# Kernel optimization log

Measured on AMD Instinct MI355X. Metric: run time of the kernel, lower is better.

## Reference

```python
import jax, jax.numpy as jnp
import numpy as np
from jax import lax

B, N, D = 2, 2048, 256
S, DC, E = 16, 4, 2
DI = E * D            # d_inner = 512
DTR = (D + 15) // 16  # dt_rank = 16


def layernorm(x, w, b):
    m = x.mean(-1, keepdims=True)
    v = ((x - m) ** 2).mean(-1, keepdims=True)
    return (x - m) / jnp.sqrt(v + 1e-5) * w + b


def mamba_block(x, in_w, conv_w, conv_b, xproj_w, dt_w, dt_b, A_log, Dp, out_w):
    # x: [B, N, D]
    xz = jnp.einsum('bnd,ed->bne', x, in_w)          # [B,N,2*DI]
    xc, z = jnp.split(xz, 2, axis=-1)
    # depthwise causal conv1d, kernel DC, left-pad DC-1
    xpad = jnp.pad(xc, ((0, 0), (DC - 1, 0), (0, 0)))
    xconv = sum(xpad[:, k:k + N, :] * conv_w[:, k] for k in range(DC)) + conv_b
    xa = jax.nn.silu(xconv)                           # [B,N,DI]
    x_dbl = jnp.einsum('bnd,ed->bne', xa, xproj_w)    # [B,N,DTR+2S]
    dt = x_dbl[..., :DTR]
    Bm = x_dbl[..., DTR:DTR + S]                      # [B,N,S]
    Cm = x_dbl[..., DTR + S:]                         # [B,N,S]
    dt = jax.nn.softplus(jnp.einsum('bnr,dr->bnd', dt, dt_w) + dt_b)  # [B,N,DI]
    A = -jnp.exp(A_log)                               # [DI,S]
    dA = jnp.exp(dt[..., None] * A)                   # [B,N,DI,S]
    dBu = dt[..., None] * Bm[:, :, None, :] * xa[..., None]

    def step(h, inp):
        dA_t, dBu_t, C_t = inp
        h = dA_t * h + dBu_t                          # [B,DI,S]
        y = jnp.einsum('bds,bs->bd', h, C_t)
        return h, y

    h0 = jnp.zeros((x.shape[0], DI, S), dtype=x.dtype)
    _, ys = lax.scan(step, h0, (dA.transpose(1, 0, 2, 3), dBu.transpose(1, 0, 2, 3), Cm.transpose(1, 0, 2)))
    y = ys.transpose(1, 0, 2) + xa * Dp               # skip D*u
    y = y * jax.nn.silu(z)
    return jnp.einsum('bnd,ed->bne', y, out_w)        # [B,N,D]


def stream_fwd(x, nw, nb, in_w, conv_w, conv_b, xproj_w, dt_w, dt_b, A_log, Dp, out_w):
    return x + mamba_block(layernorm(x, nw, nb), in_w, conv_w, conv_b, xproj_w, dt_w, dt_b, A_log, Dp, out_w)


def setup_inputs() -> dict:
    key = jax.random.key(0)
    ks = jax.random.split(key, 24)
    s = 0.02
    inp = {
        'edge_features': jax.random.normal(ks[0], (B, N, D), jnp.float32),
        'blob_features': jax.random.normal(ks[1], (B, N, D), jnp.float32),
        'spectral_features': jax.random.normal(ks[2], (B, N, D), jnp.float32),
        'norm_w': jnp.ones((3, D)),
        'norm_b': jnp.zeros((3, D)),
        'in_w': jax.random.normal(ks[3], (3, 2 * DI, D)) * s,
        'conv_w': jax.random.normal(ks[4], (3, DI, DC)) * s,
        'conv_b': jnp.zeros((3, DI)),
        'xproj_w': jax.random.normal(ks[5], (3, DTR + 2 * S, DI)) * s,
        'dt_w': jax.random.normal(ks[6], (3, DI, DTR)) * s,
        'dt_b': jax.random.uniform(ks[7], (3, DI), minval=-4.0, maxval=-2.0),
        'A_log': jnp.tile(jnp.log(jnp.arange(1, S + 1, dtype=jnp.float32)), (3, DI, 1)),
        'Dp': jnp.ones((3, DI)),
        'out_w': jax.random.normal(ks[8], (3, D, DI)) * s,
        'temperature': jnp.ones((1,)) * 0.1,
        'agg_w1': jax.random.normal(ks[9], (D, 3 * D)) * s,
        'agg_b1': jnp.zeros((D,)),
        'agg_w2': jax.random.normal(ks[10], (3, D)) * s,
        'agg_b2': jnp.zeros((3,)),
        'proj_w': jax.random.normal(ks[11], (D, 3 * D)) * s,
        'proj_b': jnp.zeros((D,)),
    }
    return inp


def reference(edge_features, blob_features, spectral_features, norm_w, norm_b, in_w,
              conv_w, conv_b, xproj_w, dt_w, dt_b, A_log, Dp, out_w, temperature,
              agg_w1, agg_b1, agg_w2, agg_b2, proj_w, proj_b):
    streams = jnp.stack([edge_features, blob_features, spectral_features])  # [3,B,N,D]
    proc = jax.vmap(stream_fwd)(streams, norm_w, norm_b, in_w, conv_w, conv_b,
                                xproj_w, dt_w, dt_b, A_log, Dp, out_w)      # [3,B,N,D]
    edge_p, blob_p, spec_p = proc[0], proc[1], proc[2]
    multi = jnp.concatenate([edge_p, blob_p, spec_p], axis=-1)              # [B,N,3D]
    pooled = multi.mean(axis=1, keepdims=True)                              # [B,1,3D]
    h = jax.nn.gelu(jnp.einsum('bne,de->bnd', pooled, agg_w1) + agg_b1)
    coeffs = jax.nn.softmax(jnp.einsum('bnd,kd->bnk', h, agg_w2) + agg_b2, axis=-1)
    coeffs = jax.nn.softmax(coeffs / (temperature + 1e-6), axis=-1)         # [B,1,3]
    weighted = (coeffs[:, :, 0:1] * edge_p + coeffs[:, :, 1:2] * blob_p +
                coeffs[:, :, 2:3] * spec_p)
    out = jnp.einsum('bne,de->bnd', multi, proj_w) + proj_b + weighted
    return out  # dropout is identity in eval
```

## Files before the change

kernel.cpp:

```cpp
#include <hip/hip_runtime.h>
#include <hip/hip_bf16.h>

#define NB 2
#define NN 2048
#define ND 256
#define NS 16
#define NDC 4
#define NDI 512
#define NDTR 16
#define LCH 64
#define NCH 32

typedef __hip_bfloat16 bf16;
typedef __attribute__((ext_vector_type(8))) __bf16 bf16x8;
typedef __attribute__((ext_vector_type(4))) float f32x4;

__device__ __forceinline__ float b2f(bf16 h) { return __bfloat162float(h); }

__device__ __forceinline__ void dec8(const uint4 u, float w[8]) {
    union { unsigned u; float f; } c;
    c.u = u.x << 16;          w[0] = c.f;
    c.u = u.x & 0xffff0000u;  w[1] = c.f;
    c.u = u.y << 16;          w[2] = c.f;
    c.u = u.y & 0xffff0000u;  w[3] = c.f;
    c.u = u.z << 16;          w[4] = c.f;
    c.u = u.z & 0xffff0000u;  w[5] = c.f;
    c.u = u.w << 16;          w[6] = c.f;
    c.u = u.w & 0xffff0000u;  w[7] = c.f;
}

struct CvtArgs { const void* s[21]; };
__device__ __constant__ const int seg_cum[22] = {
    0, 1048576, 2097152, 3145728, 3146496, 3147264, 3933696, 3939840,
    3941376, 4015104, 4039680, 4041216, 4065792, 4067328, 4460544, 4460545,
    4657153, 4657409, 4658177, 4658180, 4854788, 4855044 };
__device__ __constant__ const int seg_dst[21] = {
    0,        1048576,  2097152,  4847616, 4848384, 3145728, 4841472, 4849152, 4325376,
    4399104,  4850688,  4423680,  4852224, 3932160, 4855056, 4448256, 4853760, 4854016,
    4854784,  4644864,  4854800 };

__global__ __launch_bounds__(256) void k_convert(CvtArgs a, int* __restrict__ flag,
                                                 bf16* __restrict__ dst,
                                                 float* __restrict__ pooled)
{
    int idx = blockIdx.x * 256 + threadIdx.x;
    unsigned v0 = ((const unsigned*)a.s[3])[0];
    int f = ((v0 & 0xFFFFu) == 0u) ? 1 : 0;
    if (idx == 0) flag[0] = f;
    if (idx < 1536) pooled[idx] = 0.0f;
    if (idx >= 4855044) return;
    int seg = 0;
    #pragma unroll
    for (int i = 1; i < 21; i++) if (idx >= seg_cum[i]) seg = i;
    int off = idx - seg_cum[seg];
    bf16 v;
    if (f) v = __float2bfloat16(((const float*)a.s[seg])[off]);
    else   v = ((const bf16*)a.s[seg])[off];
    dst[seg_dst[seg] + off] = v;
}

__global__ __launch_bounds__(256) void k_layernorm(
    const bf16* __restrict__ e, const bf16* __restrict__ bl, const bf16* __restrict__ sp,
    const bf16* __restrict__ nw, const bf16* __restrict__ nb, bf16* __restrict__ xn)
{
    int row = blockIdx.x;
    int sb = row >> 11, n = row & (NN - 1);
    int s = sb >> 1, b = sb & 1;
    const bf16* xin = (s == 0) ? e : ((s == 1) ? bl : sp);
    int t = threadIdx.x;
    float v = b2f(xin[((b << 11) + n) * ND + t]);
    float s1 = v, s2 = v * v;
    #pragma unroll
    for (int m = 1; m < 64; m <<= 1) { s1 += __shfl_xor(s1, m); s2 += __shfl_xor(s2, m); }
    __shared__ float r1[4], r2[4];
    int w = t >> 6;
    if ((t & 63) == 0) { r1[w] = s1; r2[w] = s2; }
    __syncthreads();
    float mean = (r1[0] + r1[1] + r1[2] + r1[3]) * (1.0f / ND);
    float ms   = (r2[0] + r2[1] + r2[2] + r2[3]) * (1.0f / ND);
    float inv = rsqrtf(ms - mean * mean + 1e-5f);
    float wv = b2f(nw[s * ND + t]), bv = b2f(nb[s * ND + t]);
    xn[row * ND + t] = __float2bfloat16((v - mean) * inv * wv + bv);
}

__global__ __launch_bounds__(256) void k_inproj_t(
    const bf16* __restrict__ xn, const bf16* __restrict__ in_w,
    bf16* __restrict__ xc, bf16* __restrict__ z)
{
    __shared__ bf16 As[128 * 72];
    __shared__ bf16 Bs[128 * 72];
    int bid = blockIdx.x;
    int bm = bid >> 3, bn = bid & 7;
    int m0 = bm * 128, e0 = bn * 128;
    int s = m0 >> 12;
    const bf16* W = in_w + (size_t)s * (2 * NDI) * ND;
    int t = threadIdx.x;
    int w = t >> 6, l = t & 63;
    int wm = w >> 1, wn = w & 1;
    int quad = l >> 4, lan = l & 15;
    f32x4 acc[4][4];
    #pragma unroll
    for (int mi = 0; mi < 4; mi++)
        #pragma unroll
        for (int j = 0; j < 4; j++) acc[mi][j] = (f32x4){0.f, 0.f, 0.f, 0.f};
    for (int kc0 = 0; kc0 < 256; kc0 += 64) {
        __syncthreads();
        #pragma unroll
        for (int i = 0; i < 4; i++) {
            int li = i * 256 + t;
            int row = li >> 3, col = (li & 7) * 8;
            *(uint4*)&As[row * 72 + col] =
                *(const uint4*)(xn + (size_t)(m0 + row) * ND + kc0 + col);
        }
        #pragma unroll
        for (int i = 0; i < 4; i++) {
            int li = i * 256 + t;
            int row = li >> 3, col = (li & 7) * 8;
            *(uint4*)&Bs[row * 72 + col] =
                *(const uint4*)(W + (size_t)(e0 + row) * ND + kc0 + col);
        }
        __syncthreads();
        #pragma unroll
        for (int kc = 0; kc < 64; kc += 32) {
            bf16x8 af[4], bf[4];
            #pragma unroll
            for (int mi = 0; mi < 4; mi++)
                af[mi] = *(const bf16x8*)&As[(wm * 64 + mi * 16 + lan) * 72 + kc + quad * 8];
            #pragma unroll
            for (int j = 0; j < 4; j++)
                bf[j] = *(const bf16x8*)&Bs[(wn * 64 + j * 16 + lan) * 72 + kc + quad * 8];
            #pragma unroll
            for (int mi = 0; mi < 4; mi++)
                #pragma unroll
                for (int j = 0; j < 4; j++)
                    acc[mi][j] = __builtin_amdgcn_mfma_f32_16x16x32_bf16(af[mi], bf[j], acc[mi][j], 0, 0, 0);
        }
    }
    #pragma unroll
    for (int mi = 0; mi < 4; mi++) {
        #pragma unroll
        for (int j = 0; j < 4; j++) {
            int e = e0 + wn * 64 + j * 16 + lan;
            bf16* dst = (e < NDI) ? xc : z;
            int ec = e & (NDI - 1);
            #pragma unroll
            for (int r = 0; r < 4; r++) {
                int m = m0 + wm * 64 + mi * 16 + quad * 4 + r;
                dst[(size_t)m * NDI + ec] = __float2bfloat16(acc[mi][j][r]);
            }
        }
    }
}

__global__ __launch_bounds__(256) void k_conv(
    const bf16* __restrict__ xc, const bf16* __restrict__ conv_w,
    const bf16* __restrict__ conv_b, bf16* __restrict__ xa)
{
    int idx = blockIdx.x * 256 + threadIdx.x;
    int d8 = (idx & 63) * 8;
    int rn = idx >> 6;
    int n = rn & (NN - 1);
    int sb = rn >> 11;
    int s = sb >> 1;
    const uint4* cwp = (const uint4*)(conv_w + ((size_t)s * NDI + d8) * NDC);
    float cwf[32];
    dec8(cwp[0], cwf); dec8(cwp[1], cwf + 8); dec8(cwp[2], cwf + 16); dec8(cwp[3], cwf + 24);
    float bias[8];
    dec8(*(const uint4*)(conv_b + (size_t)s * NDI + d8), bias);
    size_t g = (size_t)rn * NDI + d8;
    float xv[4][8];
    #pragma unroll
    for (int tau = 0; tau < 4; tau++) {
        if (n >= tau) dec8(*(const uint4*)(xc + g - (size_t)tau * NDI), xv[tau]);
        else
            #pragma unroll
            for (int j = 0; j < 8; j++) xv[tau][j] = 0.0f;
    }
    union { bf16 h[8]; uint4 u; } o;
    #pragma unroll
    for (int j = 0; j < 8; j++) {
        float a = bias[j];
        #pragma unroll
        for (int k = 0; k < 4; k++) a += cwf[j * 4 + k] * xv[3 - k][j];
        a = a / (1.0f + __expf(-a));
        o.h[j] = __float2bfloat16(a);
    }
    *(uint4*)(xa + g) = o.u;
}

__global__ __launch_bounds__(256) void k_xproj_t(
    const bf16* __restrict__ xa, const bf16* __restrict__ xproj_w,
    float* __restrict__ xdbl)
{
    __shared__ bf16 As[128 * 72];
    __shared__ bf16 Bs[48 * 72];
    int bm = blockIdx.x;
    int m0 = bm * 128;
    int s = m0 >> 12;
    const bf16* W = xproj_w + (size_t)s * 48 * NDI;
    int t = threadIdx.x;
    int w = t >> 6, l = t & 63;
    int quad = l >> 4, lan = l & 15;
    f32x4 acc[2][3];
    #pragma unroll
    for (int mi = 0; mi < 2; mi++)
        #pragma unroll
        for (int j = 0; j < 3; j++) acc[mi][j] = (f32x4){0.f, 0.f, 0.f, 0.f};
    for (int kc0 = 0; kc0 < 512; kc0 += 64) {
        __syncthreads();
        #pragma unroll
        for (int i = 0; i < 4; i++) {
            int li = i * 256 + t;
            int row = li >> 3, col = (li & 7) * 8;
            *(uint4*)&As[row * 72 + col] =
                *(const uint4*)(xa + (size_t)(m0 + row) * NDI + kc0 + col);
        }
        {
            int li = t;
            if (li < 384) {
                int row = li >> 3, col = (li & 7) * 8;
                *(uint4*)&Bs[row * 72 + col] =
                    *(const uint4*)(W + (size_t)row * NDI + kc0 + col);
            }
            int li2 = 256 + t;
            if (li2 < 384) {
                int row = li2 >> 3, col = (li2 & 7) * 8;
                *(uint4*)&Bs[row * 72 + col] =
                    *(const uint4*)(W + (size_t)row * NDI + kc0 + col);
            }
        }
        __syncthreads();
        #pragma unroll
        for (int kc = 0; kc < 64; kc += 32) {
            bf16x8 af[2], bf[3];
            #pragma unroll
            for (int mi = 0; mi < 2; mi++)
                af[mi] = *(const bf16x8*)&As[(w * 32 + mi * 16 + lan) * 72 + kc + quad * 8];
            #pragma unroll
            for (int j = 0; j < 3; j++)
                bf[j] = *(const bf16x8*)&Bs[(j * 16 + lan) * 72 + kc + quad * 8];
            #pragma unroll
            for (int mi = 0; mi < 2; mi++)
                #pragma unroll
                for (int j = 0; j < 3; j++)
                    acc[mi][j] = __builtin_amdgcn_mfma_f32_16x16x32_bf16(af[mi], bf[j], acc[mi][j], 0, 0, 0);
        }
    }
    #pragma unroll
    for (int mi = 0; mi < 2; mi++) {
        #pragma unroll
        for (int j = 0; j < 3; j++) {
            int e = j * 16 + lan;
            #pragma unroll
            for (int r = 0; r < 4; r++) {
                int m = m0 + w * 32 + mi * 16 + quad * 4 + r;
                xdbl[(size_t)m * 48 + e] = acc[mi][j][r];
            }
        }
    }
}

__global__ __launch_bounds__(256) void k_dt(
    const float* __restrict__ xdbl, const bf16* __restrict__ dt_w,
    const bf16* __restrict__ dt_b, bf16* __restrict__ dt)
{
    __shared__ float xs[4][16];
    int row0 = blockIdx.x * 4;
    int s = row0 >> 12;
    int t = threadIdx.x;
    if (t < 64) xs[t >> 4][t & 15] = xdbl[(size_t)(row0 + (t >> 4)) * 48 + (t & 15)];
    __syncthreads();
    for (int dd = 0; dd < 2; dd++) {
        int d = t + dd * 256;
        const uint4* wp = (const uint4*)(dt_w + ((size_t)s * NDI + d) * NDTR);
        float w[16]; dec8(wp[0], w); dec8(wp[1], w + 8);
        float bias = b2f(dt_b[s * NDI + d]);
        #pragma unroll
        for (int r = 0; r < 4; r++) {
            float a = bias;
            #pragma unroll
            for (int j = 0; j < 16; j++) a += w[j] * xs[r][j];
            a = (a > 20.0f) ? a : log1pf(__expf(a));
            dt[(size_t)(row0 + r) * NDI + d] = __float2bfloat16(a);
        }
    }
}

__global__ __launch_bounds__(256) void k_scan1(
    const bf16* __restrict__ dt, const bf16* __restrict__ xa,
    const bf16* __restrict__ A_log, const float* __restrict__ xdbl,
    float* __restrict__ Hend, float* __restrict__ Pprod)
{
    __shared__ float Bs[LCH * NS];
    int bid = blockIdx.x;
    int sb = bid / (NCH * 2);
    int rem = bid % (NCH * 2);
    int chunk = rem >> 1, dg = rem & 1;
    int s = sb >> 1;
    int t = threadIdx.x;
    int d = dg * 256 + t;
    int n0 = chunk * LCH;
    size_t rowbase = (size_t)sb * NN;
    {
        int row = t >> 2, q = t & 3;
        ((float4*)Bs)[t] = ((const float4*)(xdbl + (rowbase + n0 + row) * 48 + 16))[q];
    }
    float A[16];
    {
        const uint4* ap = (const uint4*)(A_log + ((size_t)s * NDI + d) * NS);
        float al[8]; dec8(ap[0], al);
        #pragma unroll
        for (int i = 0; i < 8; i++) A[i] = -__expf(al[i]);
        dec8(ap[1], al);
        #pragma unroll
        for (int i = 0; i < 8; i++) A[8 + i] = -__expf(al[i]);
    }
    __syncthreads();
    float h[16], P[16];
    #pragma unroll
    for (int i = 0; i < 16; i++) { h[i] = 0.0f; P[i] = 1.0f; }
    const bf16* dtp = dt + (rowbase + n0) * NDI + d;
    const bf16* xap = xa + (rowbase + n0) * NDI + d;
    for (int nl = 0; nl < LCH; nl += 4) {
        float dtv[4], xav[4];
        #pragma unroll
        for (int j = 0; j < 4; j++) {
            dtv[j] = b2f(dtp[(size_t)(nl + j) * NDI]);
            xav[j] = b2f(xap[(size_t)(nl + j) * NDI]);
        }
        #pragma unroll
        for (int j = 0; j < 4; j++) {
            float bcom = dtv[j] * xav[j];
            const float4* br = (const float4*)&Bs[(nl + j) * NS];
            float4 b0 = br[0], b1 = br[1], b2 = br[2], b3 = br[3];
            float bv[16] = {b0.x,b0.y,b0.z,b0.w,b1.x,b1.y,b1.z,b1.w,
                            b2.x,b2.y,b2.z,b2.w,b3.x,b3.y,b3.z,b3.w};
            #pragma unroll
            for (int st = 0; st < 16; st++) {
                float dA = __expf(dtv[j] * A[st]);
                h[st] = dA * h[st] + bcom * bv[st];
                P[st] *= dA;
            }
        }
    }
    size_t base = ((size_t)(chunk * 6 + sb) * NS) * NDI + d;
    #pragma unroll
    for (int st = 0; st < 16; st++) {
        Hend[base + (size_t)st * NDI] = h[st];
        Pprod[base + (size_t)st * NDI] = P[st];
    }
}

__global__ __launch_bounds__(256) void k_scomb(float* __restrict__ Hend, const float* __restrict__ Pprod)
{
    int idx = blockIdx.x * 256 + threadIdx.x;
    int sb = idx >> 13;
    int rem = idx & 8191;
    int st = rem >> 9, d = rem & 511;
    float h = 0.0f;
    const size_t stride = (size_t)6 * NS * NDI;
    size_t g = ((size_t)sb * NS + st) * NDI + d;
    #pragma unroll 4
    for (int c = 0; c < NCH; c++) {
        float He = Hend[g], Pp = Pprod[g];
        Hend[g] = h;
        h = He + Pp * h;
        g += stride;
    }
}

__global__ __launch_bounds__(256) void k_scan2(
    const bf16* __restrict__ dt, const bf16* __restrict__ xa, const bf16* __restrict__ z,
    const float* __restrict__ xdbl,
    const bf16* __restrict__ A_log, const bf16* __restrict__ Dp,
    const float* __restrict__ Hstart, bf16* __restrict__ y)
{
    __shared__ float Bs[LCH * NS], Cs[LCH * NS];
    int bid = blockIdx.x;
    int sb = bid / (NCH * 2);
    int rem = bid % (NCH * 2);
    int chunk = rem >> 1, dg = rem & 1;
    int s = sb >> 1;
    int t = threadIdx.x;
    int d = dg * 256 + t;
    int n0 = chunk * LCH;
    size_t rowbase = (size_t)sb * NN;
    {
        int row = t >> 2, q = t & 3;
        ((float4*)Bs)[t] = ((const float4*)(xdbl + (rowbase + n0 + row) * 48 + 16))[q];
        ((float4*)Cs)[t] = ((const float4*)(xdbl + (rowbase + n0 + row) * 48 + 32))[q];
    }
    float A[16];
    {
        const uint4* ap = (const uint4*)(A_log + ((size_t)s * NDI + d) * NS);
        float al[8]; dec8(ap[0], al);
        #pragma unroll
        for (int i = 0; i < 8; i++) A[i] = -__expf(al[i]);
        dec8(ap[1], al);
        #pragma unroll
        for (int i = 0; i < 8; i++) A[8 + i] = -__expf(al[i]);
    }
    float Dpv = b2f(Dp[s * NDI + d]);
    float h[16];
    {
        size_t base = ((size_t)(chunk * 6 + sb) * NS) * NDI + d;
        #pragma unroll
        for (int st = 0; st < 16; st++) h[st] = Hstart[base + (size_t)st * NDI];
    }
    __syncthreads();
    const bf16* dtp = dt + (rowbase + n0) * NDI + d;
    const bf16* xap = xa + (rowbase + n0) * NDI + d;
    const bf16* zp  = z  + (rowbase + n0) * NDI + d;
    bf16* yp = y + (rowbase + n0) * NDI + d;
    for (int nl = 0; nl < LCH; nl += 4) {
        float dtv[4], xav[4], zv[4];
        #pragma unroll
        for (int j = 0; j < 4; j++) {
            dtv[j] = b2f(dtp[(size_t)(nl + j) * NDI]);
            xav[j] = b2f(xap[(size_t)(nl + j) * NDI]);
            zv[j]  = b2f(zp [(size_t)(nl + j) * NDI]);
        }
        #pragma unroll
        for (int j = 0; j < 4; j++) {
            float bcom = dtv[j] * xav[j];
            const float4* br = (const float4*)&Bs[(nl + j) * NS];
            const float4* cr = (const float4*)&Cs[(nl + j) * NS];
            float4 b0 = br[0], b1 = br[1], b2 = br[2], b3 = br[3];
            float4 c0 = cr[0], c1 = cr[1], c2 = cr[2], c3 = cr[3];
            float bv[16] = {b0.x,b0.y,b0.z,b0.w,b1.x,b1.y,b1.z,b1.w,
                            b2.x,b2.y,b2.z,b2.w,b3.x,b3.y,b3.z,b3.w};
            float cv[16] = {c0.x,c0.y,c0.z,c0.w,c1.x,c1.y,c1.z,c1.w,
                            c2.x,c2.y,c2.z,c2.w,c3.x,c3.y,c3.z,c3.w};
            float yacc = 0.0f;
            #pragma unroll
            for (int st = 0; st < 16; st++) {
                float dA = __expf(dtv[j] * A[st]);
                h[st] = dA * h[st] + bcom * bv[st];
                yacc += h[st] * cv[st];
            }
            float yv = yacc + xav[j] * Dpv;
            float zz = zv[j];
            yv *= zz / (1.0f + __expf(-zz));
            yp[(size_t)(nl + j) * NDI] = __float2bfloat16(yv);
        }
    }
}

__global__ __launch_bounds__(256) void k_outproj_t(
    const bf16* __restrict__ y, const bf16* __restrict__ out_w,
    const bf16* __restrict__ e_, const bf16* __restrict__ bl, const bf16* __restrict__ sp,
    bf16* __restrict__ proc)
{
    __shared__ bf16 As[128 * 72];
    __shared__ bf16 Bs[64 * 72];
    int bid = blockIdx.x;
    int bm = bid >> 2, bn = bid & 3;
    int m0 = bm * 128, e0 = bn * 64;
    int s = m0 >> 12;
    const bf16* W = out_w + (size_t)s * ND * NDI;
    int t = threadIdx.x;
    int w = t >> 6, l = t & 63;
    int quad = l >> 4, lan = l & 15;
    f32x4 acc[2][4];
    #pragma unroll
    for (int mi = 0; mi < 2; mi++)
        #pragma unroll
        for (int j = 0; j < 4; j++) acc[mi][j] = (f32x4){0.f, 0.f, 0.f, 0.f};
    for (int kc0 = 0; kc0 < 512; kc0 += 64) {
        __syncthreads();
        #pragma unroll
        for (int i = 0; i < 4; i++) {
            int li = i * 256 + t;
            int row = li >> 3, col = (li & 7) * 8;
            *(uint4*)&As[row * 72 + col] =
                *(const uint4*)(y + (size_t)(m0 + row) * NDI + kc0 + col);
        }
        #pragma unroll
        for (int i = 0; i < 2; i++) {
            int li = i * 256 + t;
            int row = li >> 3, col = (li & 7) * 8;
            *(uint4*)&Bs[row * 72 + col] =
                *(const uint4*)(W + (size_t)(e0 + row) * NDI + kc0 + col);
        }
        __syncthreads();
        #pragma unroll
        for (int kc = 0; kc < 64; kc += 32) {
            bf16x8 af[2], bf[4];
            #pragma unroll
            for (int mi = 0; mi < 2; mi++)
                af[mi] = *(const bf16x8*)&As[(w * 32 + mi * 16 + lan) * 72 + kc + quad * 8];
            #pragma unroll
            for (int j = 0; j < 4; j++)
                bf[j] = *(const bf16x8*)&Bs[(j * 16 + lan) * 72 + kc + quad * 8];
            #pragma unroll
            for (int mi = 0; mi < 2; mi++)
                #pragma unroll
                for (int j = 0; j < 4; j++)
                    acc[mi][j] = __builtin_amdgcn_mfma_f32_16x16x32_bf16(af[mi], bf[j], acc[mi][j], 0, 0, 0);
        }
    }
    const bf16* xin = (s == 0) ? e_ : ((s == 1) ? bl : sp);
    #pragma unroll
    for (int mi = 0; mi < 2; mi++) {
        #pragma unroll
        for (int j = 0; j < 4; j++) {
            int e = e0 + j * 16 + lan;
            #pragma unroll
            for (int r = 0; r < 4; r++) {
                int m = m0 + w * 32 + mi * 16 + quad * 4 + r;
                int b = (m >> 11) & 1, n = m & (NN - 1);
                float res = b2f(xin[((size_t)(b * NN + n)) * ND + e]);
                proc[(size_t)m * ND + e] = __float2bfloat16(acc[mi][j][r] + res);
            }
        }
    }
}

__global__ __launch_bounds__(256) void k_pool2(const bf16* __restrict__ proc, float* __restrict__ pooled)
{
    int bid = blockIdx.x;
    int sb = bid / 8, chunk = bid % 8;
    int s = sb >> 1, b = sb & 1;
    int t = threadIdx.x;
    size_t base = ((size_t)sb * NN + chunk * 256) * ND + t;
    float acc = 0.0f;
    for (int r = 0; r < 256; r++) acc += b2f(proc[base + (size_t)r * ND]);
    atomicAdd(&pooled[b * 768 + s * 256 + t], acc);
}

__global__ __launch_bounds__(256) void k_coeff(
    const float* __restrict__ pooled,
    const bf16* __restrict__ agg_w1, const bf16* __restrict__ agg_b1,
    const bf16* __restrict__ agg_w2, const bf16* __restrict__ agg_b2,
    const bf16* __restrict__ temp, float* __restrict__ coeffs)
{
    __shared__ float hb[256];
    __shared__ float lg[3];
    int t = threadIdx.x;
    for (int b = 0; b < NB; b++) {
        float dot = 0.0f;
        const uint4* wp = (const uint4*)(agg_w1 + (size_t)t * 768);
        for (int k8 = 0; k8 < 96; k8++) {
            float w[8]; dec8(wp[k8], w);
            const float* pp = pooled + b * 768 + k8 * 8;
            #pragma unroll
            for (int j = 0; j < 8; j++) dot += w[j] * pp[j];
        }
        float x = b2f(agg_b1[t]) + dot * (1.0f / NN);
        float inner = 0.7978845608028654f * (x + 0.044715f * x * x * x);
        hb[t] = 0.5f * x * (1.0f + tanhf(inner));
        __syncthreads();
        if (t < 3) {
            float l = b2f(agg_b2[t]);
            const bf16* w2 = agg_w2 + t * 256;
            for (int d2 = 0; d2 < 256; d2++) l += b2f(w2[d2]) * hb[d2];
            lg[t] = l;
        }
        __syncthreads();
        if (t == 0) {
            float m = fmaxf(lg[0], fmaxf(lg[1], lg[2]));
            float e0 = __expf(lg[0] - m), e1 = __expf(lg[1] - m), e2 = __expf(lg[2] - m);
            float iS = 1.0f / (e0 + e1 + e2);
            float c0 = e0 * iS, c1 = e1 * iS, c2 = e2 * iS;
            float tt = b2f(temp[0]) + 1e-6f;
            float m2 = fmaxf(c0, fmaxf(c1, c2)) / tt;
            e0 = __expf(c0 / tt - m2); e1 = __expf(c1 / tt - m2); e2 = __expf(c2 / tt - m2);
            iS = 1.0f / (e0 + e1 + e2);
            coeffs[b * 3 + 0] = e0 * iS;
            coeffs[b * 3 + 1] = e1 * iS;
            coeffs[b * 3 + 2] = e2 * iS;
        }
        __syncthreads();
    }
}

__global__ __launch_bounds__(256) void k_final_t(
    const bf16* __restrict__ proc, const bf16* __restrict__ proj_w,
    const bf16* __restrict__ proj_b, const float* __restrict__ coeffs,
    const int* __restrict__ flag, void* __restrict__ out)
{
    __shared__ bf16 As[128 * 72];
    __shared__ bf16 Bs[64 * 72];
    int bid = blockIdx.x;
    int bm = bid >> 2, bn = bid & 3;
    int m0 = bm * 128, e0 = bn * 64;
    int b = m0 >> 11;
    int nbase = m0 & (NN - 1);
    int t = threadIdx.x;
    int w = t >> 6, l = t & 63;
    int quad = l >> 4, lan = l & 15;
    f32x4 acc[2][4];
    #pragma unroll
    for (int mi = 0; mi < 2; mi++)
        #pragma unroll
        for (int j = 0; j < 4; j++) acc[mi][j] = (f32x4){0.f, 0.f, 0.f, 0.f};
    for (int kc0 = 0; kc0 < 768; kc0 += 64) {
        int sA = kc0 >> 8, kd0 = kc0 & 255;
        const bf16* Asrc = proc + ((size_t)(sA * NB + b) * NN + nbase) * ND + kd0;
        __syncthreads();
        #pragma unroll
        for (int i = 0; i < 4; i++) {
            int li = i * 256 + t;
            int row = li >> 3, col = (li & 7) * 8;
            *(uint4*)&As[row * 72 + col] = *(const uint4*)(Asrc + (size_t)row * ND + col);
        }
        #pragma unroll
        for (int i = 0; i < 2; i++) {
            int li = i * 256 + t;
            int row = li >> 3, col = (li & 7) * 8;
            *(uint4*)&Bs[row * 72 + col] =
                *(const uint4*)(proj_w + (size_t)(e0 + row) * 768 + kc0 + col);
        }
        __syncthreads();
        #pragma unroll
        for (int kc = 0; kc < 64; kc += 32) {
            bf16x8 af[2], bf[4];
            #pragma unroll
            for (int mi = 0; mi < 2; mi++)
                af[mi] = *(const bf16x8*)&As[(w * 32 + mi * 16 + lan) * 72 + kc + quad * 8];
            #pragma unroll
            for (int j = 0; j < 4; j++)
                bf[j] = *(const bf16x8*)&Bs[(j * 16 + lan) * 72 + kc + quad * 8];
            #pragma unroll
            for (int mi = 0; mi < 2; mi++)
                #pragma unroll
                for (int j = 0; j < 4; j++)
                    acc[mi][j] = __builtin_amdgcn_mfma_f32_16x16x32_bf16(af[mi], bf[j], acc[mi][j], 0, 0, 0);
        }
    }
    float c0 = coeffs[b * 3], c1 = coeffs[b * 3 + 1], c2 = coeffs[b * 3 + 2];
    int f = flag[0];
    #pragma unroll
    for (int mi = 0; mi < 2; mi++) {
        #pragma unroll
        for (int j = 0; j < 4; j++) {
            int e = e0 + j * 16 + lan;
            float pb = b2f(proj_b[e]);
            #pragma unroll
            for (int r = 0; r < 4; r++) {
                int m = m0 + w * 32 + mi * 16 + quad * 4 + r;
                int n = m & (NN - 1);
                size_t pbase = ((size_t)b * NN + n) * ND + e;
                float wres = c0 * b2f(proc[pbase])
                           + c1 * b2f(proc[pbase + (size_t)1 * NB * NN * ND])
                           + c2 * b2f(proc[pbase + (size_t)2 * NB * NN * ND]);
                float v = acc[mi][j][r] + pb + wres;
                if (f) ((float*)out)[(size_t)m * ND + e] = v;
                else   ((bf16*)out)[(size_t)m * ND + e] = __float2bfloat16(v);
            }
        }
    }
}

extern "C" void kernel_launch(void* const* d_in, const int* in_sizes, int n_in,
                              void* d_out, int out_size, void* d_ws, size_t ws_size,
                              hipStream_t stream)
{
    char* w8 = (char*)d_ws;
    int*   flagp   = (int*)(w8);
    bf16*  cvt     = (bf16*)(w8 + 16);
    bf16*  xn      = (bf16*)(w8 + 9710160);
    bf16*  xcb     = (bf16*)(w8 + 16001616);
    bf16*  zb      = (bf16*)(w8 + 28584528);
    bf16*  xab     = (bf16*)(w8 + 41167440);
    bf16*  dtb     = (bf16*)(w8 + 53750352);
    float* xdblb   = (float*)(w8 + 66333264);
    float* pooledb = (float*)(w8 + 68692560);
    float* coeffsb = (float*)(w8 + 68698704);
    float* Pprodb  = (float*)(w8 + 68698736);
    float* Hendb   = (float*)xn;
    bf16*  procb   = xn;

    const bf16* c_edge   = cvt + 0;
    const bf16* c_blob   = cvt + 1048576;
    const bf16* c_spec   = cvt + 2097152;
    const bf16* c_inw    = cvt + 3145728;
    const bf16* c_outw   = cvt + 3932160;
    const bf16* c_xpw    = cvt + 4325376;
    const bf16* c_dtw    = cvt + 4399104;
    const bf16* c_alog   = cvt + 4423680;
    const bf16* c_agg1   = cvt + 4448256;
    const bf16* c_prjw   = cvt + 4644864;
    const bf16* c_convw  = cvt + 4841472;
    const bf16* c_nrmw   = cvt + 4847616;
    const bf16* c_nrmb   = cvt + 4848384;
    const bf16* c_convb  = cvt + 4849152;
    const bf16* c_dtb    = cvt + 4850688;
    const bf16* c_dp     = cvt + 4852224;
    const bf16* c_agb1   = cvt + 4853760;
    const bf16* c_agw2   = cvt + 4854016;
    const bf16* c_agb2   = cvt + 4854784;
    const bf16* c_prjb   = cvt + 4854800;
    const bf16* c_temp   = cvt + 4855056;

    CvtArgs ca;
    for (int i = 0; i < 21; i++) ca.s[i] = d_in[i];
    k_convert<<<(4855044 + 255) / 256, 256, 0, stream>>>(ca, flagp, cvt, pooledb);

    k_layernorm<<<6 * NN, 256, 0, stream>>>(c_edge, c_blob, c_spec, c_nrmw, c_nrmb, xn);
    k_inproj_t<<<96 * 8, 256, 0, stream>>>(xn, c_inw, xcb, zb);
    k_conv<<<6 * NN * NDI / 8 / 256, 256, 0, stream>>>(xcb, c_convw, c_convb, xab);
    k_xproj_t<<<96, 256, 0, stream>>>(xab, c_xpw, xdblb);
    k_dt<<<3072, 256, 0, stream>>>(xdblb, c_dtw, c_dtb, dtb);
    k_scan1<<<6 * NCH * 2, 256, 0, stream>>>(dtb, xab, c_alog, xdblb, Hendb, Pprodb);
    k_scomb<<<192, 256, 0, stream>>>(Hendb, Pprodb);
    k_scan2<<<6 * NCH * 2, 256, 0, stream>>>(dtb, xab, zb, xdblb, c_alog, c_dp, Hendb, xcb);
    k_outproj_t<<<96 * 4, 256, 0, stream>>>(xcb, c_outw, c_edge, c_blob, c_spec, procb);
    k_pool2<<<48, 256, 0, stream>>>(procb, pooledb);
    k_coeff<<<1, 256, 0, stream>>>(pooledb, c_agg1, c_agb1, c_agw2, c_agb2, c_temp, coeffsb);
    k_final_t<<<32 * 4, 256, 0, stream>>>(procb, c_prjw, c_prjb, coeffsb, flagp, d_out);
}
```

Baseline: 357.9 us.

## Split-K x-projection, halve scan chunk length, fuse pooling into out-projection

The x-projection GEMM is split four ways along K with smaller 64-row tiles, so it runs as 768 blocks instead of 96. The dt kernel now sums the partial results and writes the B/C columns of xdbl. The scan chunk length is halved to double the block count of the scan kernels, and Hend/Pprod move to dedicated workspace. The pooling sum is folded into the out-projection epilogue using shared and global atomics, removing a kernel. The costs are extra partial-buffer traffic, a longer sequential chunk-combine step, and atomic contention.

Measured after the change: 337.3 us. -5.8%, faster.

```diff
diff --git a/kernel.cpp b/kernel.cpp
--- a/kernel.cpp
+++ b/kernel.cpp
@@ -8,8 +8,8 @@
 #define NDC 4
 #define NDI 512
 #define NDTR 16
-#define LCH 64
-#define NCH 32
+#define LCH 32
+#define NCH 64
 
 typedef __hip_bfloat16 bf16;
 typedef __attribute__((ext_vector_type(8))) __bf16 bf16x8;
@@ -190,26 +190,25 @@
 
 __global__ __launch_bounds__(256) void k_xproj_t(
     const bf16* __restrict__ xa, const bf16* __restrict__ xproj_w,
-    float* __restrict__ xdbl)
-{
-    __shared__ bf16 As[128 * 72];
+    float* __restrict__ xpart)
+{
+    __shared__ bf16 As[64 * 72];
     __shared__ bf16 Bs[48 * 72];
-    int bm = blockIdx.x;
-    int m0 = bm * 128;
+    int bid = blockIdx.x;
+    int bm = bid >> 2, ks = bid & 3;
+    int m0 = bm * 64;
     int s = m0 >> 12;
     const bf16* W = xproj_w + (size_t)s * 48 * NDI;
     int t = threadIdx.x;
     int w = t >> 6, l = t & 63;
     int quad = l >> 4, lan = l & 15;
-    f32x4 acc[2][3];
-    #pragma unroll
-    for (int mi = 0; mi < 2; mi++)
-        #pragma unroll
-        for (int j = 0; j < 3; j++) acc[mi][j] = (f32x4){0.f, 0.f, 0.f, 0.f};
-    for (int kc0 = 0; kc0 < 512; kc0 += 64) {
-        __syncthreads();
-        #pragma unroll
-        for (int i = 0; i < 4; i++) {
+    f32x4 acc[3];
+    #pragma unroll
+    for (int j = 0; j < 3; j++) acc[j] = (f32x4){0.f, 0.f, 0.f, 0.f};
+    for (int kc0 = ks * 128; kc0 < ks * 128 + 128; kc0 += 64) {
+        __syncthreads();
+        #pragma unroll
+        for (int i = 0; i < 2; i++) {
             int li = i * 256 + t;
             int row = li >> 3, col = (li & 7) * 8;
             *(uint4*)&As[row * 72 + col] =
@@ -232,44 +231,44 @@
         __syncthreads();
         #pragma unroll
         for (int kc = 0; kc < 64; kc += 32) {
-            bf16x8 af[2], bf[3];
-            #pragma unroll
-            for (int mi = 0; mi < 2; mi++)
-                af[mi] = *(const bf16x8*)&As[(w * 32 + mi * 16 + lan) * 72 + kc + quad * 8];
-            #pragma unroll
-            for (int j = 0; j < 3; j++)
-                bf[j] = *(const bf16x8*)&Bs[(j * 16 + lan) * 72 + kc + quad * 8];
-            #pragma unroll
-            for (int mi = 0; mi < 2; mi++)
-                #pragma unroll
-                for (int j = 0; j < 3; j++)
-                    acc[mi][j] = __builtin_amdgcn_mfma_f32_16x16x32_bf16(af[mi], bf[j], acc[mi][j], 0, 0, 0);
-        }
-    }
-    #pragma unroll
-    for (int mi = 0; mi < 2; mi++) {
-        #pragma unroll
-        for (int j = 0; j < 3; j++) {
-            int e = j * 16 + lan;
-            #pragma unroll
-            for (int r = 0; r < 4; r++) {
-                int m = m0 + w * 32 + mi * 16 + quad * 4 + r;
-                xdbl[(size_t)m * 48 + e] = acc[mi][j][r];
+            bf16x8 af = *(const bf16x8*)&As[(w * 16 + lan) * 72 + kc + quad * 8];
+            #pragma unroll
+            for (int j = 0; j < 3; j++) {
+                bf16x8 bf = *(const bf16x8*)&Bs[(j * 16 + lan) * 72 + kc + quad * 8];
+                acc[j] = __builtin_amdgcn_mfma_f32_16x16x32_bf16(af, bf, acc[j], 0, 0, 0);
             }
         }
     }
-}
-
-__global__ __launch_bounds__(256) void k_dt(
-    const float* __restrict__ xdbl, const bf16* __restrict__ dt_w,
-    const bf16* __restrict__ dt_b, bf16* __restrict__ dt)
-{
-    __shared__ float xs[4][16];
+    float* dst = xpart + (size_t)ks * (12288 * 48);
+    #pragma unroll
+    for (int j = 0; j < 3; j++) {
+        int e = j * 16 + lan;
+        #pragma unroll
+        for (int r = 0; r < 4; r++) {
+            int m = m0 + w * 16 + quad * 4 + r;
+            dst[(size_t)m * 48 + e] = acc[j][r];
+        }
+    }
+}
+
+__global__ __launch_bounds__(256) void k_dt2(
+    const float* __restrict__ xpart, const bf16* __restrict__ dt_w,
+    const bf16* __restrict__ dt_b, float* __restrict__ xdbl, bf16* __restrict__ dt)
+{
+    __shared__ float xs[4][48];
     int row0 = blockIdx.x * 4;
     int s = row0 >> 12;
     int t = threadIdx.x;
-    if (t < 64) xs[t >> 4][t & 15] = xdbl[(size_t)(row0 + (t >> 4)) * 48 + (t & 15)];
+    if (t < 192) {
+        int r = t / 48, e = t % 48;
+        size_t base = (size_t)(row0 + r) * 48 + e;
+        const size_t seg = (size_t)12288 * 48;
+        float v = xpart[base] + xpart[base + seg] + xpart[base + 2 * seg] + xpart[base + 3 * seg];
+        xs[r][e] = v;
+        if (e >= 16) xdbl[base] = v;
+    }
     __syncthreads();
+    #pragma unroll
     for (int dd = 0; dd < 2; dd++) {
         int d = t + dd * 256;
         const uint4* wp = (const uint4*)(dt_w + ((size_t)s * NDI + d) * NDTR);
@@ -301,7 +300,7 @@
     int d = dg * 256 + t;
     int n0 = chunk * LCH;
     size_t rowbase = (size_t)sb * NN;
-    {
+    if (t < 128) {
         int row = t >> 2, q = t & 3;
         ((float4*)Bs)[t] = ((const float4*)(xdbl + (rowbase + n0 + row) * 48 + 16))[q];
     }
@@ -385,10 +384,13 @@
     int d = dg * 256 + t;
     int n0 = chunk * LCH;
     size_t rowbase = (size_t)sb * NN;
-    {
+    if (t < 128) {
         int row = t >> 2, q = t & 3;
         ((float4*)Bs)[t] = ((const float4*)(xdbl + (rowbase + n0 + row) * 48 + 16))[q];
-        ((float4*)Cs)[t] = ((const float4*)(xdbl + (rowbase + n0 + row) * 48 + 32))[q];
+    } else {
+        int t2 = t - 128;
+        int row = t2 >> 2, q = t2 & 3;
+        ((float4*)Cs)[t2] = ((const float4*)(xdbl + (rowbase + n0 + row) * 48 + 32))[q];
     }
     float A[16];
     {
@@ -449,10 +451,11 @@
 __global__ __launch_bounds__(256) void k_outproj_t(
     const bf16* __restrict__ y, const bf16* __restrict__ out_w,
     const bf16* __restrict__ e_, const bf16* __restrict__ bl, const bf16* __restrict__ sp,
-    bf16* __restrict__ proc)
+    bf16* __restrict__ proc, float* __restrict__ pooled)
 {
     __shared__ bf16 As[128 * 72];
     __shared__ bf16 Bs[64 * 72];
+    __shared__ float colsum[64];
     int bid = blockIdx.x;
     int bm = bid >> 2, bn = bid & 3;
     int m0 = bm * 128, e0 = bn * 64;
@@ -499,33 +502,29 @@
                     acc[mi][j] = __builtin_amdgcn_mfma_f32_16x16x32_bf16(af[mi], bf[j], acc[mi][j], 0, 0, 0);
         }
     }
+    if (t < 64) colsum[t] = 0.0f;
+    __syncthreads();
     const bf16* xin = (s == 0) ? e_ : ((s == 1) ? bl : sp);
+    int b = (m0 >> 11) & 1;
     #pragma unroll
     for (int mi = 0; mi < 2; mi++) {
         #pragma unroll
         for (int j = 0; j < 4; j++) {
             int e = e0 + j * 16 + lan;
+            float ps = 0.0f;
             #pragma unroll
             for (int r = 0; r < 4; r++) {
                 int m = m0 + w * 32 + mi * 16 + quad * 4 + r;
-                int b = (m >> 11) & 1, n = m & (NN - 1);
-                float res = b2f(xin[((size_t)(b * NN + n)) * ND + e]);
-                proc[(size_t)m * ND + e] = __float2bfloat16(acc[mi][j][r] + res);
+                int n = m & (NN - 1);
+                float v = acc[mi][j][r] + b2f(xin[((size_t)(b * NN + n)) * ND + e]);
+                proc[(size_t)m * ND + e] = __float2bfloat16(v);
+                ps += v;
             }
-        }
-    }
-}
-
-__global__ __launch_bounds__(256) void k_pool2(const bf16* __restrict__ proc, float* __restrict__ pooled)
-{
-    int bid = blockIdx.x;
-    int sb = bid / 8, chunk = bid % 8;
-    int s = sb >> 1, b = sb & 1;
-    int t = threadIdx.x;
-    size_t base = ((size_t)sb * NN + chunk * 256) * ND + t;
-    float acc = 0.0f;
-    for (int r = 0; r < 256; r++) acc += b2f(proc[base + (size_t)r * ND]);
-    atomicAdd(&pooled[b * 768 + s * 256 + t], acc);
+            atomicAdd(&colsum[j * 16 + lan], ps);
+        }
+    }
+    __syncthreads();
+    if (t < 64) atomicAdd(&pooled[b * 768 + s * 256 + e0 + t], colsum[t]);
 }
 
 __global__ __launch_bounds__(256) void k_coeff(
@@ -667,8 +666,9 @@
     float* xdblb   = (float*)(w8 + 66333264);
     float* pooledb = (float*)(w8 + 68692560);
     float* coeffsb = (float*)(w8 + 68698704);
-    float* Pprodb  = (float*)(w8 + 68698736);
-    float* Hendb   = (float*)xn;
+    float* Hendb   = (float*)(w8 + 68698736);
+    float* Pprodb  = (float*)(w8 + 81281648);
+    float* xpartb  = (float*)(w8 + 93864560);
     bf16*  procb   = xn;
 
     const bf16* c_edge   = cvt + 0;
@@ -700,13 +700,12 @@
     k_layernorm<<<6 * NN, 256, 0, stream>>>(c_edge, c_blob, c_spec, c_nrmw, c_nrmb, xn);
     k_inproj_t<<<96 * 8, 256, 0, stream>>>(xn, c_inw, xcb, zb);
     k_conv<<<6 * NN * NDI / 8 / 256, 256, 0, stream>>>(xcb, c_convw, c_convb, xab);
-    k_xproj_t<<<96, 256, 0, stream>>>(xab, c_xpw, xdblb);
-    k_dt<<<3072, 256, 0, stream>>>(xdblb, c_dtw, c_dtb, dtb);
+    k_xproj_t<<<192 * 4, 256, 0, stream>>>(xab, c_xpw, xpartb);
+    k_dt2<<<3072, 256, 0, stream>>>(xpartb, c_dtw, c_dtb, xdblb, dtb);
     k_scan1<<<6 * NCH * 2, 256, 0, stream>>>(dtb, xab, c_alog, xdblb, Hendb, Pprodb);
     k_scomb<<<192, 256, 0, stream>>>(Hendb, Pprodb);
     k_scan2<<<6 * NCH * 2, 256, 0, stream>>>(dtb, xab, zb, xdblb, c_alog, c_dp, Hendb, xcb);
-    k_outproj_t<<<96 * 4, 256, 0, stream>>>(xcb, c_outw, c_edge, c_blob, c_spec, procb);
-    k_pool2<<<48, 256, 0, stream>>>(procb, pooledb);
+    k_outproj_t<<<96 * 4, 256, 0, stream>>>(xcb, c_outw, c_edge, c_blob, c_spec, procb, pooledb);
     k_coeff<<<1, 256, 0, stream>>>(pooledb, c_agg1, c_agb1, c_agw2, c_agb2, c_temp, coeffsb);
     k_final_t<<<32 * 4, 256, 0, stream>>>(procb, c_prjw, c_prjb, coeffsb, flagp, d_out);
 }
```
